# Performance work log

Measured on AMD Instinct MI355X. Metric: run time of the kernel, lower is better.

## Reference

```python
import math
import jax, jax.numpy as jnp
import numpy as np

EPS = 1e-6
MAX_SCALE_LOG = math.log(100.0)

def rms_norm(x, scale, eps=EPS):
    # x * scale / rms(x), reduction over last dim
    ms = jnp.mean(jnp.square(x), axis=-1, keepdims=True)
    return x * (scale * jax.lax.rsqrt(ms + eps))

def axial_rope_theta(pos, n_heads, d_head, dtype):
    # freqs: linspace in log-space from pi to 10*pi, reshaped to [n_heads, d_head//4]
    f = np.exp(np.linspace(math.log(math.pi), math.log(10.0 * math.pi),
                           n_heads * d_head // 4 + 1)[:-1])
    freqs = jnp.asarray(f.reshape(d_head // 4, n_heads).T, dtype)  # [h, e/4]
    theta_h = pos[:, :, None, 0:1] * freqs  # [n, l, h, e/4]
    theta_w = pos[:, :, None, 1:2] * freqs  # [n, l, h, e/4]
    theta = jnp.concatenate([theta_h, theta_w], axis=-1)  # [n, l, h, e/2]
    return theta.transpose(0, 2, 1, 3)  # [n, h, l, e/2]

def apply_rotary(x, theta):
    d = theta.shape[-1]
    x1, x2, x3 = x[..., :d], x[..., d:2 * d], x[..., 2 * d:]
    cos, sin = jnp.cos(theta), jnp.sin(theta)
    return jnp.concatenate([x1 * cos - x2 * sin, x2 * cos + x1 * sin, x3], axis=-1)

def setup_inputs() -> dict:
    key = jax.random.key(0)
    ks = jax.random.split(key, 8)
    n, l, d_model, d_head = 2, 2048, 1024, 64
    n_heads = d_model // d_head
    x = jax.random.normal(ks[0], (n, l, d_model), jnp.float32)
    pos = jax.random.uniform(ks[1], (n, l, 2), jnp.float32)
    cond = jax.random.normal(ks[2], (n, 1, d_model), jnp.float32)
    # params (torch uses zero-init for w_cond/w_out; small random for a non-degenerate baseline)
    w_cond = jax.random.normal(ks[3], (d_model, d_model), jnp.float32) * 0.02
    w_qkv = jax.random.normal(ks[4], (d_model, 3 * d_model), jnp.float32) * (d_model ** -0.5)
    qk_scale = jnp.full((n_heads,), math.log(10.0), jnp.float32)
    w_out = jax.random.normal(ks[5], (d_model, d_model), jnp.float32) * 0.02
    return {"x": x, "pos": pos, "cond": cond, "w_cond": w_cond,
            "w_qkv": w_qkv, "qk_scale": qk_scale, "w_out": w_out}

def reference(x, pos, cond, w_cond, w_qkv, qk_scale, w_out):
    n, l, d_model = x.shape
    h = qk_scale.shape[0]
    e = d_model // h
    # AdaRMSNorm: scale = linear(cond) + 1
    xn = rms_norm(x, cond @ w_cond + 1.0)
    # QKV projection
    q, k, v = jnp.split(xn @ w_qkv, 3, axis=-1)
    to_heads = lambda t: t.reshape(n, l, h, e).transpose(0, 2, 1, 3)  # [n,h,l,e]
    q, k, v = to_heads(q), to_heads(k), to_heads(v)
    # QKNorm: per-head learned scale, rms over head dim
    s = jnp.exp(0.5 * jnp.minimum(qk_scale, MAX_SCALE_LOG) - 0.25 * math.log(e))
    q = rms_norm(q, s[:, None, None])
    k = rms_norm(k, s[:, None, None])
    # Axial RoPE
    theta = axial_rope_theta(pos, h, e, x.dtype)
    q = apply_rotary(q, theta)
    k = apply_rotary(k, theta)
    # SDPA (no mask)
    attn = jax.nn.softmax(jnp.einsum('nhqe,nhke->nhqk', q, k) / math.sqrt(e), axis=-1)
    o = jnp.einsum('nhqk,nhke->nhqe', attn, v)
    o = o.transpose(0, 2, 1, 3).reshape(n, l, d_model)
    return o @ w_out
```

## Files before the change

kernel.cpp:

```cpp
#include <hip/hip_runtime.h>

typedef unsigned short u16;
typedef unsigned int u32;
typedef short s16x8 __attribute__((ext_vector_type(8)));
typedef short s16x4 __attribute__((ext_vector_type(4)));
typedef float f32x4 __attribute__((ext_vector_type(4)));
typedef u32 u32x2 __attribute__((ext_vector_type(2)));

#define AS1 __attribute__((address_space(1)))
#define AS3 __attribute__((address_space(3)))

__device__ __forceinline__ float bf2f(u16 u) {
    union { unsigned int i; float f; } x; x.i = ((unsigned int)u) << 16; return x.f;
}
__device__ __forceinline__ u16 f2bf(float f) {
    union { float f; unsigned int i; } x; x.f = f;
    unsigned int r = (x.i + 0x7FFFu + ((x.i >> 16) & 1u)) >> 16;
    return (u16)r;
}
__device__ __forceinline__ void storeOut(u16* p, float v) { *p = f2bf(v); }
__device__ __forceinline__ void storeOut(float* p, float v) { *p = v; }
__device__ __forceinline__ float loadIn(const void* p, size_t i, int isf32) {
    return isf32 ? ((const float*)p)[i] : bf2f(((const u16*)p)[i]);
}
__device__ __forceinline__ float fexp2(float x) {
#if __has_builtin(__builtin_amdgcn_exp2f)
    return __builtin_amdgcn_exp2f(x);
#else
    return exp2f(x);
#endif
}
__device__ __forceinline__ u32 pack_bf(float a, float b) {
    u32 ua = __float_as_uint(a) + 0x8000u;
    u32 ub = __float_as_uint(b) + 0x8000u;
    return __builtin_amdgcn_perm(ub, ua, 0x07060302u);
}

__global__ __launch_bounds__(256) void detect_dtype(const u16* __restrict__ x,
                                                    int* __restrict__ flag) {
    __shared__ int cnt[4];
    const int tid = threadIdx.x;
    int c = 0;
    #pragma unroll
    for (int i = 0; i < 4; ++i) {
        const u16 u = x[tid * 4 + i];
        const int e = (u >> 7) & 0xFF;
        c += (e >= 101 && e <= 135) ? 1 : 0;
    }
    #pragma unroll
    for (int m = 1; m < 64; m <<= 1) c += __shfl_xor(c, m, 64);
    if ((tid & 63) == 0) cnt[tid >> 6] = c;
    __syncthreads();
    if (tid == 0) {
        const int t = cnt[0] + cnt[1] + cnt[2] + cnt[3];
        *flag = (t < 800) ? 1 : 0;
    }
}

__global__ __launch_bounds__(256) void cond_gemv(const void* __restrict__ cond,
                                                 const void* __restrict__ w,
                                                 float* __restrict__ out,
                                                 const int* __restrict__ flag) {
    const int isf32 = *flag;
    const int d  = blockIdx.x * 256 + threadIdx.x;
    const int n  = blockIdx.y;
    const int k0 = blockIdx.z * 64;
    float acc = 0.f;
    #pragma unroll 8
    for (int k = 0; k < 64; ++k)
        acc += loadIn(cond, n * 1024 + k0 + k, isf32) *
               loadIn(w, (size_t)(k0 + k) * 1024 + d, isf32);
    atomicAdd(out + n * 1024 + d, acc);
}

__global__ __launch_bounds__(256) void rmsnorm_x(const void* __restrict__ x,
                                                 const float* __restrict__ scl,
                                                 u16* __restrict__ xn,
                                                 const int* __restrict__ flag) {
    const int isf32 = *flag;
    const int tok = blockIdx.x;
    const int n = tok >> 11;
    u16* orow = xn + (size_t)tok * 1024;
    const int base = threadIdx.x * 4;
    float f0, f1, f2, f3;
    if (isf32) {
        const float4 v = *(const float4*)((const float*)x + (size_t)tok * 1024 + base);
        f0 = v.x; f1 = v.y; f2 = v.z; f3 = v.w;
    } else {
        s16x4 uv = *(const s16x4*)((const u16*)x + (size_t)tok * 1024 + base);
        f0 = bf2f((u16)uv[0]); f1 = bf2f((u16)uv[1]); f2 = bf2f((u16)uv[2]); f3 = bf2f((u16)uv[3]);
    }
    float ss = f0 * f0 + f1 * f1 + f2 * f2 + f3 * f3;
    #pragma unroll
    for (int m = 1; m < 64; m <<= 1) ss += __shfl_xor(ss, m, 64);
    __shared__ float red[4];
    const int wave = threadIdx.x >> 6, lane = threadIdx.x & 63;
    if (lane == 0) red[wave] = ss;
    __syncthreads();
    float ms = (red[0] + red[1] + red[2] + red[3]) * (1.f / 1024.f);
    float rinv = rsqrtf(ms + 1e-6f);
    orow[base + 0] = f2bf(f0 * (scl[n * 1024 + base + 0] + 1.f) * rinv);
    orow[base + 1] = f2bf(f1 * (scl[n * 1024 + base + 1] + 1.f) * rinv);
    orow[base + 2] = f2bf(f2 * (scl[n * 1024 + base + 2] + 1.f) * rinv);
    orow[base + 3] = f2bf(f3 * (scl[n * 1024 + base + 3] + 1.f) * rinv);
}

__global__ __launch_bounds__(256) void transpose_bf(const void* __restrict__ src,
                                                    u16* __restrict__ dst, int R, int C,
                                                    const int* __restrict__ flag) {
    const int isf32 = *flag;
    __shared__ u16 t[32][33];
    const int c0 = blockIdx.x * 32, r0 = blockIdx.y * 32;
    const int tx = threadIdx.x & 31, ty = threadIdx.x >> 5;
    #pragma unroll
    for (int i = 0; i < 4; ++i)
        t[ty + i * 8][tx] = f2bf(loadIn(src, (size_t)(r0 + ty + i * 8) * C + c0 + tx, isf32));
    __syncthreads();
    #pragma unroll
    for (int i = 0; i < 4; ++i)
        dst[(size_t)(c0 + ty + i * 8) * R + r0 + tx] = t[tx][ty + i * 8];
}

template <typename OutT>
__global__ __launch_bounds__(256) void gemm_bt(const u16* __restrict__ A,
                                               const u16* __restrict__ BT,
                                               OutT* __restrict__ C, int Nn, int K) {
    __shared__ u16 As[128 * 32];
    __shared__ u16 Bs[128 * 32];
    const int tid = threadIdx.x;
    const int wave = tid >> 6, lane = tid & 63;
    const int l15 = lane & 15, quad = lane >> 4;
    const int bm0 = blockIdx.y * 128, bn0 = blockIdx.x * 128;
    const int wr = wave >> 1, wc = wave & 1;
    f32x4 acc[4][4] = {};
    const int srow = lane >> 2;
    const int g = (lane & 3) ^ (srow & 3);
    for (int bk = 0; bk < K; bk += 32) {
        __syncthreads();
        #pragma unroll
        for (int p = 0; p < 2; ++p) {
            const int rowl = p * 64 + wave * 16 + srow;
            __builtin_amdgcn_global_load_lds(
                (const AS1 void*)(A + (size_t)(bm0 + rowl) * K + bk + g * 8),
                (AS3 void*)(As + (p * 64 + wave * 16) * 32), 16, 0, 0);
            __builtin_amdgcn_global_load_lds(
                (const AS1 void*)(BT + (size_t)(bn0 + rowl) * K + bk + g * 8),
                (AS3 void*)(Bs + (p * 64 + wave * 16) * 32), 16, 0, 0);
        }
        __syncthreads();
        s16x8 af[4], bfr[4];
        #pragma unroll
        for (int mt = 0; mt < 4; ++mt) {
            const int r = wr * 64 + mt * 16 + l15;
            af[mt] = *(const s16x8*)(As + r * 32 + ((quad ^ (r & 3)) << 3));
        }
        #pragma unroll
        for (int nt = 0; nt < 4; ++nt) {
            const int r = wc * 64 + nt * 16 + l15;
            bfr[nt] = *(const s16x8*)(Bs + r * 32 + ((quad ^ (r & 3)) << 3));
        }
        #pragma unroll
        for (int mt = 0; mt < 4; ++mt)
            #pragma unroll
            for (int nt = 0; nt < 4; ++nt)
                acc[mt][nt] = __builtin_amdgcn_mfma_f32_16x16x32_bf16(af[mt], bfr[nt], acc[mt][nt], 0, 0, 0);
    }
    #pragma unroll
    for (int mt = 0; mt < 4; ++mt)
        #pragma unroll
        for (int nt = 0; nt < 4; ++nt)
            #pragma unroll
            for (int r = 0; r < 4; ++r) {
                const int row = bm0 + wr * 64 + mt * 16 + quad * 4 + r;
                const int col = bn0 + wc * 64 + nt * 16 + l15;
                storeOut(C + (size_t)row * Nn + col, acc[mt][nt][r]);
            }
}

template <typename OutT>
__global__ __launch_bounds__(256) void gemm_bt64(const u16* __restrict__ A,
                                                 const u16* __restrict__ BT,
                                                 OutT* __restrict__ C, int Nn, int K) {
    __shared__ u16 As[128 * 32];
    __shared__ u16 Bs[64 * 32];
    const int tid = threadIdx.x;
    const int wave = tid >> 6, lane = tid & 63;
    const int l15 = lane & 15, quad = lane >> 4;
    const int bm0 = blockIdx.y * 128, bn0 = blockIdx.x * 64;
    f32x4 acc[2][4] = {};
    const int srow = lane >> 2;
    const int g = (lane & 3) ^ (srow & 3);
    for (int bk = 0; bk < K; bk += 32) {
        __syncthreads();
        #pragma unroll
        for (int p = 0; p < 2; ++p) {
            const int rowl = p * 64 + wave * 16 + srow;
            __builtin_amdgcn_global_load_lds(
                (const AS1 void*)(A + (size_t)(bm0 + rowl) * K + bk + g * 8),
                (AS3 void*)(As + (p * 64 + wave * 16) * 32), 16, 0, 0);
        }
        {
            const int rowb = wave * 16 + srow;
            __builtin_amdgcn_global_load_lds(
                (const AS1 void*)(BT + (size_t)(bn0 + rowb) * K + bk + g * 8),
                (AS3 void*)(Bs + (wave * 16) * 32), 16, 0, 0);
        }
        __syncthreads();
        s16x8 af[2], bfr[4];
        #pragma unroll
        for (int mt = 0; mt < 2; ++mt) {
            const int r = wave * 32 + mt * 16 + l15;
            af[mt] = *(const s16x8*)(As + r * 32 + ((quad ^ (r & 3)) << 3));
        }
        #pragma unroll
        for (int nt = 0; nt < 4; ++nt) {
            const int r = nt * 16 + l15;
            bfr[nt] = *(const s16x8*)(Bs + r * 32 + ((quad ^ (r & 3)) << 3));
        }
        #pragma unroll
        for (int mt = 0; mt < 2; ++mt)
            #pragma unroll
            for (int nt = 0; nt < 4; ++nt)
                acc[mt][nt] = __builtin_amdgcn_mfma_f32_16x16x32_bf16(af[mt], bfr[nt], acc[mt][nt], 0, 0, 0);
    }
    #pragma unroll
    for (int mt = 0; mt < 2; ++mt)
        #pragma unroll
        for (int nt = 0; nt < 4; ++nt)
            #pragma unroll
            for (int r = 0; r < 4; ++r) {
                const int row = bm0 + wave * 32 + mt * 16 + quad * 4 + r;
                const int col = bn0 + nt * 16 + l15;
                storeOut(C + (size_t)row * Nn + col, acc[mt][nt][r]);
            }
}

__global__ __launch_bounds__(256) void qkv_head(const u16* __restrict__ qkv,
                                                const void* __restrict__ pos,
                                                const void* __restrict__ qk_scale,
                                                u16* __restrict__ q_ws,
                                                u16* __restrict__ k_ws,
                                                u16* __restrict__ vtg,
                                                const int* __restrict__ flag) {
    const int isf32 = *flag;
    const int nh = blockIdx.y;
    const int n = nh >> 4, h = nh & 15;
    const int l0 = blockIdx.x * 64;
    const int tid = threadIdx.x;
    const int wave = tid >> 6, lane = tid & 63;

    const float qs = loadIn(qk_scale, h, isf32);
    const float s = __expf(0.5f * fminf(qs, 4.605170186f) - 1.039720771f);
    const float qmul = s * s * 0.125f * 1.44269504089f;
    const int j = lane & 31;
    const float t = (float)((j & 15) * 16 + h);
    const float freq = 3.14159265358979f * __expf(t * (2.302585093f / 256.f));
    const int pj = j >> 4;

    #pragma unroll 2
    for (int it = 0; it < 16; ++it) {
        const int l = l0 + wave * 16 + it;
        const int tok = n * 2048 + l;
        const u16* row = qkv + (size_t)tok * 3072;
        float qv = bf2f(row[h * 64 + lane]);
        float kv = bf2f(row[1024 + h * 64 + lane]);
        float q2 = qv * qv, k2 = kv * kv;
        #pragma unroll
        for (int m = 1; m < 64; m <<= 1) { q2 += __shfl_xor(q2, m, 64); k2 += __shfl_xor(k2, m, 64); }
        float qn = qv * rsqrtf(q2 * (1.f / 64.f) + 1e-6f) * qmul;
        float kn = kv * rsqrtf(k2 * (1.f / 64.f) + 1e-6f);
        const float p = loadIn(pos, tok * 2 + pj, isf32);
        const float th = p * freq;
        const float c = __cosf(th), sn = __sinf(th);
        const float pq = __shfl_xor(qn, 32, 64);
        const float pk = __shfl_xor(kn, 32, 64);
        float qr, kr;
        if (lane < 32) { qr = qn * c - pq * sn; kr = kn * c - pk * sn; }
        else           { qr = qn * c + pq * sn; kr = kn * c + pk * sn; }
        const size_t oidx = ((size_t)nh * 2048 + l) * 64 + lane;
        q_ws[oidx] = f2bf(qr);
        k_ws[oidx] = f2bf(kr);
    }

    __shared__ u16 tbuf[64][65];
    const u16* vsrc = qkv + (size_t)(n * 2048 + l0) * 3072 + 2048 + h * 64;
    #pragma unroll
    for (int it = 0; it < 16; ++it) {
        const int idx = it * 256 + tid;
        const int r = idx >> 6, c = idx & 63;
        tbuf[r][c] = vsrc[(size_t)r * 3072 + c];
    }
    __syncthreads();
    u16* dst = vtg + (size_t)nh * 131072 + l0;
    #pragma unroll
    for (int it = 0; it < 16; ++it) {
        const int idx = it * 256 + tid;
        const int er = idx >> 6, lc = idx & 63;
        dst[(size_t)er * 2048 + lc] = tbuf[lc][er];
    }
}

__global__ __launch_bounds__(256, 3) void attn6(const u16* __restrict__ Q,
                                                const u16* __restrict__ K,
                                                const u16* __restrict__ Vtg,
                                                float* __restrict__ Opart,
                                                float* __restrict__ lpart) {
    __shared__ u16 Ks[2][64 * 64];
    __shared__ u16 Vt[2][64 * 64];
    __shared__ u16 Ps[4][32 * 72];
    const int nh = blockIdx.y;
    const int q0 = blockIdx.x * 128;
    const int ks = blockIdx.z;
    const int kb0 = ks * 1024;
    const int tid = threadIdx.x;
    const int wave = tid >> 6, lane = tid & 63;
    const int l15 = lane & 15, quad = lane >> 4;
    const size_t hb = (size_t)nh * 2048 * 64;
    const u16* Vbase = Vtg + (size_t)nh * 131072;
    const int dr0 = tid >> 3;
    const int dd  = tid & 7;

    s16x8 qf[2][2];
    #pragma unroll
    for (int qg = 0; qg < 2; ++qg)
        #pragma unroll
        for (int kc = 0; kc < 2; ++kc)
            qf[qg][kc] = *(const s16x8*)(Q + hb + (size_t)(q0 + wave * 32 + qg * 16 + l15) * 64 + kc * 32 + quad * 8);

    f32x4 Oacc[2][4] = {};
    float lacc[2] = {0.f, 0.f};
    u16* Pw = Ps[wave];

    #pragma unroll
    for (int it = 0; it < 2; ++it) {
        const int row = it * 32 + dr0;
        const int g = dd ^ (row & 7);
        __builtin_amdgcn_global_load_lds(
            (const AS1 void*)(K + hb + (size_t)(kb0 + row) * 64 + g * 8),
            (AS3 void*)(Ks[0] + (it * 256 + wave * 64) * 8), 16, 0, 0);
        __builtin_amdgcn_global_load_lds(
            (const AS1 void*)(Vbase + (size_t)row * 2048 + kb0 + g * 8),
            (AS3 void*)(Vt[0] + (it * 256 + wave * 64) * 8), 16, 0, 0);
    }
    __syncthreads();

    for (int i = 0; i < 16; ++i) {
        const int cur = i & 1;
        const int kb = kb0 + i * 64;
        if (i < 15) {
            const int nxt = cur ^ 1;
            const int kbn = kb + 64;
            #pragma unroll
            for (int it = 0; it < 2; ++it) {
                const int row = it * 32 + dr0;
                const int g = dd ^ (row & 7);
                __builtin_amdgcn_global_load_lds(
                    (const AS1 void*)(K + hb + (size_t)(kbn + row) * 64 + g * 8),
                    (AS3 void*)(Ks[nxt] + (it * 256 + wave * 64) * 8), 16, 0, 0);
                __builtin_amdgcn_global_load_lds(
                    (const AS1 void*)(Vbase + (size_t)row * 2048 + kbn + g * 8),
                    (AS3 void*)(Vt[nxt] + (it * 256 + wave * 64) * 8), 16, 0, 0);
            }
        }

        f32x4 S[2][4];
        #pragma unroll
        for (int qg = 0; qg < 2; ++qg)
            #pragma unroll
            for (int kt = 0; kt < 4; ++kt) {
                S[qg][kt][0] = -15.f; S[qg][kt][1] = -15.f;
                S[qg][kt][2] = -15.f; S[qg][kt][3] = -15.f;
            }
        #pragma unroll
        for (int kt = 0; kt < 4; ++kt) {
            const int r = kt * 16 + l15;
            #pragma unroll
            for (int kc = 0; kc < 2; ++kc) {
                const s16x8 kf = *(const s16x8*)(Ks[cur] + r * 64 + (((kc * 4 + quad) ^ (r & 7)) << 3));
                S[0][kt] = __builtin_amdgcn_mfma_f32_16x16x32_bf16(kf, qf[0][kc], S[0][kt], 0, 0, 0);
                S[1][kt] = __builtin_amdgcn_mfma_f32_16x16x32_bf16(kf, qf[1][kc], S[1][kt], 0, 0, 0);
            }
        }

        #pragma unroll
        for (int qg = 0; qg < 2; ++qg) {
            float rs = 0.f;
            #pragma unroll
            for (int kt = 0; kt < 4; ++kt) {
                const float e0 = fexp2(S[qg][kt][0]);
                const float e1 = fexp2(S[qg][kt][1]);
                const float e2 = fexp2(S[qg][kt][2]);
                const float e3 = fexp2(S[qg][kt][3]);
                rs += (e0 + e1) + (e2 + e3);
                u32x2 pk2;
                pk2[0] = pack_bf(e0, e1);
                pk2[1] = pack_bf(e2, e3);
                *(u32x2*)(Pw + (qg * 16 + l15) * 72 + kt * 16 + quad * 4) = pk2;
            }
            lacc[qg] += rs;
        }

        #pragma unroll
        for (int kc = 0; kc < 2; ++kc) {
            const s16x8 pf0 = *(const s16x8*)(Pw + l15 * 72 + kc * 32 + quad * 8);
            const s16x8 pf1 = *(const s16x8*)(Pw + (16 + l15) * 72 + kc * 32 + quad * 8);
            #pragma unroll
            for (int nto = 0; nto < 4; ++nto) {
                const int e = nto * 16 + l15;
                const s16x8 vf = *(const s16x8*)(Vt[cur] + e * 64 + (((kc * 4 + quad) ^ (e & 7)) << 3));
                Oacc[0][nto] = __builtin_amdgcn_mfma_f32_16x16x32_bf16(pf0, vf, Oacc[0][nto], 0, 0, 0);
                Oacc[1][nto] = __builtin_amdgcn_mfma_f32_16x16x32_bf16(pf1, vf, Oacc[1][nto], 0, 0, 0);
            }
        }

        if (i < 15) __syncthreads();
    }

    #pragma unroll
    for (int qg = 0; qg < 2; ++qg) {
        lacc[qg] += __shfl_xor(lacc[qg], 16, 64);
        lacc[qg] += __shfl_xor(lacc[qg], 32, 64);
    }

    const size_t pb = ((size_t)(ks * 32 + nh)) * 2048;
    if (quad == 0) {
        #pragma unroll
        for (int qg = 0; qg < 2; ++qg)
            lpart[pb + q0 + wave * 32 + qg * 16 + l15] = lacc[qg];
    }
    #pragma unroll
    for (int qg = 0; qg < 2; ++qg)
        #pragma unroll
        for (int r = 0; r < 4; ++r) {
            const int qrow = q0 + wave * 32 + qg * 16 + quad * 4 + r;
            float* orow = Opart + (pb + qrow) * 64;
            #pragma unroll
            for (int nto = 0; nto < 4; ++nto)
                orow[nto * 16 + l15] = Oacc[qg][nto][r];
        }
}

__global__ __launch_bounds__(256) void combine_o(const float* __restrict__ Opart,
                                                 const float* __restrict__ lpart,
                                                 u16* __restrict__ O) {
    constexpr size_t HS = (size_t)32 * 2048 * 64;
    constexpr size_t LS = (size_t)32 * 2048;
    const int tok = blockIdx.x;
    const int n = tok >> 11, l = tok & 2047;
    const int idx = threadIdx.x * 4;
    const int h = idx >> 6;
    const int nh = n * 16 + h;
    const size_t base = ((size_t)nh * 2048 + l) * 64 + (idx & 63);
    const float4 a = *(const float4*)(Opart + base);
    const float4 b = *(const float4*)(Opart + HS + base);
    const float inv = 1.f / (lpart[(size_t)nh * 2048 + l] + lpart[LS + (size_t)nh * 2048 + l]);
    u16* o = O + (size_t)tok * 1024 + idx;
    o[0] = f2bf((a.x + b.x) * inv);
    o[1] = f2bf((a.y + b.y) * inv);
    o[2] = f2bf((a.z + b.z) * inv);
    o[3] = f2bf((a.w + b.w) * inv);
}

extern "C" void kernel_launch(void* const* d_in, const int* in_sizes, int n_in,
                              void* d_out, int out_size, void* d_ws, size_t ws_size,
                              hipStream_t stream) {
    const void* x        = d_in[0];
    const void* pos      = d_in[1];
    const void* cond     = d_in[2];
    const void* w_cond   = d_in[3];
    const void* w_qkv    = d_in[4];
    const void* qk_scale = d_in[5];
    const void* w_out    = d_in[6];

    char* ws = (char*)d_ws;
    constexpr size_t MB = 1048576;
    constexpr size_t OFS_SCALE = 0;
    constexpr size_t OFS_FLAG  = 8192;
    constexpr size_t OFS_WOUTT = 16384;
    constexpr size_t OFS_Q     = OFS_WOUTT + 2 * MB;
    constexpr size_t OFS_K     = OFS_Q     + 8 * MB;
    constexpr size_t OFS_VT    = OFS_K     + 8 * MB;
    constexpr size_t OFS_O     = OFS_VT    + 8 * MB;
    constexpr size_t OFS_XN    = OFS_O     + 8 * MB;
    constexpr size_t OFS_WQKVT = OFS_XN    + 8 * MB;
    constexpr size_t OFS_QKV   = OFS_WQKVT + 6 * MB;
    constexpr size_t OFS_OPART = OFS_XN;
    constexpr size_t OFS_LPART = OFS_OPART + 32 * MB;

    float* scale = (float*)(ws + OFS_SCALE);
    int*   flag  = (int*)(ws + OFS_FLAG);
    u16* xn    = (u16*)(ws + OFS_XN);
    u16* wqkvT = (u16*)(ws + OFS_WQKVT);
    u16* woutT = (u16*)(ws + OFS_WOUTT);
    u16* qkv   = (u16*)(ws + OFS_QKV);
    u16* qws   = (u16*)(ws + OFS_Q);
    u16* kws   = (u16*)(ws + OFS_K);
    u16* vtg   = (u16*)(ws + OFS_VT);
    u16* ows   = (u16*)(ws + OFS_O);
    float* opart = (float*)(ws + OFS_OPART);
    float* lpart = (float*)(ws + OFS_LPART);

    detect_dtype<<<dim3(1), 256, 0, stream>>>((const u16*)x, flag);
    hipMemsetAsync(scale, 0, 2 * 1024 * sizeof(float), stream);
    cond_gemv<<<dim3(4, 2, 16), 256, 0, stream>>>(cond, w_cond, scale, flag);
    rmsnorm_x<<<dim3(4096), 256, 0, stream>>>(x, scale, xn, flag);
    transpose_bf<<<dim3(96, 32), 256, 0, stream>>>(w_qkv, wqkvT, 1024, 3072, flag);
    transpose_bf<<<dim3(32, 32), 256, 0, stream>>>(w_out, woutT, 1024, 1024, flag);
    gemm_bt<u16><<<dim3(24, 32), 256, 0, stream>>>(xn, wqkvT, qkv, 3072, 1024);
    qkv_head<<<dim3(32, 32), 256, 0, stream>>>(qkv, pos, qk_scale, qws, kws, vtg, flag);
    attn6<<<dim3(16, 32, 2), 256, 0, stream>>>(qws, kws, vtg, opart, lpart);
    combine_o<<<dim3(4096), 256, 0, stream>>>(opart, lpart, ows);
    gemm_bt64<float><<<dim3(16, 32), 256, 0, stream>>>(ows, woutT, (float*)d_out, 1024, 1024);
}
```

Measured before the change: 246.7 us.

## Double query rows per attention block and use 128-wide GEMM for output projection

The attention kernel now gives each wave 64 query rows instead of 32, so every K/V tile loaded into shared memory feeds twice as many MFMAs. The grid is halved and occupancy is lowered to 2 blocks per CU. The output projection drops the 128x64-tile GEMM in favour of the generic 128x128 gemm_bt kernel. The cost is more register pressure and fewer blocks: the attention launch goes to 512 blocks and the output GEMM to 256, which may underfill the GPU.

```diff
diff --git a/kernel.cpp b/kernel.cpp
--- a/kernel.cpp
+++ b/kernel.cpp
@@ -177,64 +177,6 @@
             }
 }
 
-template <typename OutT>
-__global__ __launch_bounds__(256) void gemm_bt64(const u16* __restrict__ A,
-                                                 const u16* __restrict__ BT,
-                                                 OutT* __restrict__ C, int Nn, int K) {
-    __shared__ u16 As[128 * 32];
-    __shared__ u16 Bs[64 * 32];
-    const int tid = threadIdx.x;
-    const int wave = tid >> 6, lane = tid & 63;
-    const int l15 = lane & 15, quad = lane >> 4;
-    const int bm0 = blockIdx.y * 128, bn0 = blockIdx.x * 64;
-    f32x4 acc[2][4] = {};
-    const int srow = lane >> 2;
-    const int g = (lane & 3) ^ (srow & 3);
-    for (int bk = 0; bk < K; bk += 32) {
-        __syncthreads();
-        #pragma unroll
-        for (int p = 0; p < 2; ++p) {
-            const int rowl = p * 64 + wave * 16 + srow;
-            __builtin_amdgcn_global_load_lds(
-                (const AS1 void*)(A + (size_t)(bm0 + rowl) * K + bk + g * 8),
-                (AS3 void*)(As + (p * 64 + wave * 16) * 32), 16, 0, 0);
-        }
-        {
-            const int rowb = wave * 16 + srow;
-            __builtin_amdgcn_global_load_lds(
-                (const AS1 void*)(BT + (size_t)(bn0 + rowb) * K + bk + g * 8),
-                (AS3 void*)(Bs + (wave * 16) * 32), 16, 0, 0);
-        }
-        __syncthreads();
-        s16x8 af[2], bfr[4];
-        #pragma unroll
-        for (int mt = 0; mt < 2; ++mt) {
-            const int r = wave * 32 + mt * 16 + l15;
-            af[mt] = *(const s16x8*)(As + r * 32 + ((quad ^ (r & 3)) << 3));
-        }
-        #pragma unroll
-        for (int nt = 0; nt < 4; ++nt) {
-            const int r = nt * 16 + l15;
-            bfr[nt] = *(const s16x8*)(Bs + r * 32 + ((quad ^ (r & 3)) << 3));
-        }
-        #pragma unroll
-        for (int mt = 0; mt < 2; ++mt)
-            #pragma unroll
-            for (int nt = 0; nt < 4; ++nt)
-                acc[mt][nt] = __builtin_amdgcn_mfma_f32_16x16x32_bf16(af[mt], bfr[nt], acc[mt][nt], 0, 0, 0);
-    }
-    #pragma unroll
-    for (int mt = 0; mt < 2; ++mt)
-        #pragma unroll
-        for (int nt = 0; nt < 4; ++nt)
-            #pragma unroll
-            for (int r = 0; r < 4; ++r) {
-                const int row = bm0 + wave * 32 + mt * 16 + quad * 4 + r;
-                const int col = bn0 + nt * 16 + l15;
-                storeOut(C + (size_t)row * Nn + col, acc[mt][nt][r]);
-            }
-}
-
 __global__ __launch_bounds__(256) void qkv_head(const u16* __restrict__ qkv,
                                                 const void* __restrict__ pos,
                                                 const void* __restrict__ qk_scale,
@@ -300,16 +242,16 @@
     }
 }
 
-__global__ __launch_bounds__(256, 3) void attn6(const u16* __restrict__ Q,
+__global__ __launch_bounds__(256, 2) void attn7(const u16* __restrict__ Q,
                                                 const u16* __restrict__ K,
                                                 const u16* __restrict__ Vtg,
                                                 float* __restrict__ Opart,
                                                 float* __restrict__ lpart) {
     __shared__ u16 Ks[2][64 * 64];
     __shared__ u16 Vt[2][64 * 64];
-    __shared__ u16 Ps[4][32 * 72];
+    __shared__ u16 Ps[4][64 * 72];
     const int nh = blockIdx.y;
-    const int q0 = blockIdx.x * 128;
+    const int q0 = blockIdx.x * 256;
     const int ks = blockIdx.z;
     const int kb0 = ks * 1024;
     const int tid = threadIdx.x;
@@ -320,15 +262,15 @@
     const int dr0 = tid >> 3;
     const int dd  = tid & 7;
 
-    s16x8 qf[2][2];
-    #pragma unroll
-    for (int qg = 0; qg < 2; ++qg)
+    s16x8 qf[4][2];
+    #pragma unroll
+    for (int qg = 0; qg < 4; ++qg)
         #pragma unroll
         for (int kc = 0; kc < 2; ++kc)
-            qf[qg][kc] = *(const s16x8*)(Q + hb + (size_t)(q0 + wave * 32 + qg * 16 + l15) * 64 + kc * 32 + quad * 8);
-
-    f32x4 Oacc[2][4] = {};
-    float lacc[2] = {0.f, 0.f};
+            qf[qg][kc] = *(const s16x8*)(Q + hb + (size_t)(q0 + wave * 64 + qg * 16 + l15) * 64 + kc * 32 + quad * 8);
+
+    f32x4 Oacc[4][4] = {};
+    float lacc[4] = {0.f, 0.f, 0.f, 0.f};
     u16* Pw = Ps[wave];
 
     #pragma unroll
@@ -363,9 +305,9 @@
             }
         }
 
-        f32x4 S[2][4];
-        #pragma unroll
-        for (int qg = 0; qg < 2; ++qg)
+        f32x4 S[4][4];
+        #pragma unroll
+        for (int qg = 0; qg < 4; ++qg)
             #pragma unroll
             for (int kt = 0; kt < 4; ++kt) {
                 S[qg][kt][0] = -15.f; S[qg][kt][1] = -15.f;
@@ -377,13 +319,14 @@
             #pragma unroll
             for (int kc = 0; kc < 2; ++kc) {
                 const s16x8 kf = *(const s16x8*)(Ks[cur] + r * 64 + (((kc * 4 + quad) ^ (r & 7)) << 3));
-                S[0][kt] = __builtin_amdgcn_mfma_f32_16x16x32_bf16(kf, qf[0][kc], S[0][kt], 0, 0, 0);
-                S[1][kt] = __builtin_amdgcn_mfma_f32_16x16x32_bf16(kf, qf[1][kc], S[1][kt], 0, 0, 0);
-            }
-        }
-
-        #pragma unroll
-        for (int qg = 0; qg < 2; ++qg) {
+                #pragma unroll
+                for (int qg = 0; qg < 4; ++qg)
+                    S[qg][kt] = __builtin_amdgcn_mfma_f32_16x16x32_bf16(kf, qf[qg][kc], S[qg][kt], 0, 0, 0);
+            }
+        }
+
+        #pragma unroll
+        for (int qg = 0; qg < 4; ++qg) {
             float rs = 0.f;
             #pragma unroll
             for (int kt = 0; kt < 4; ++kt) {
@@ -402,14 +345,17 @@
 
         #pragma unroll
         for (int kc = 0; kc < 2; ++kc) {
-            const s16x8 pf0 = *(const s16x8*)(Pw + l15 * 72 + kc * 32 + quad * 8);
-            const s16x8 pf1 = *(const s16x8*)(Pw + (16 + l15) * 72 + kc * 32 + quad * 8);
+            s16x8 pf[4];
+            #pragma unroll
+            for (int qg = 0; qg < 4; ++qg)
+                pf[qg] = *(const s16x8*)(Pw + (qg * 16 + l15) * 72 + kc * 32 + quad * 8);
             #pragma unroll
             for (int nto = 0; nto < 4; ++nto) {
                 const int e = nto * 16 + l15;
                 const s16x8 vf = *(const s16x8*)(Vt[cur] + e * 64 + (((kc * 4 + quad) ^ (e & 7)) << 3));
-                Oacc[0][nto] = __builtin_amdgcn_mfma_f32_16x16x32_bf16(pf0, vf, Oacc[0][nto], 0, 0, 0);
-                Oacc[1][nto] = __builtin_amdgcn_mfma_f32_16x16x32_bf16(pf1, vf, Oacc[1][nto], 0, 0, 0);
+                #pragma unroll
+                for (int qg = 0; qg < 4; ++qg)
+                    Oacc[qg][nto] = __builtin_amdgcn_mfma_f32_16x16x32_bf16(pf[qg], vf, Oacc[qg][nto], 0, 0, 0);
             }
         }
 
@@ -417,7 +363,7 @@
     }
 
     #pragma unroll
-    for (int qg = 0; qg < 2; ++qg) {
+    for (int qg = 0; qg < 4; ++qg) {
         lacc[qg] += __shfl_xor(lacc[qg], 16, 64);
         lacc[qg] += __shfl_xor(lacc[qg], 32, 64);
     }
@@ -425,14 +371,14 @@
     const size_t pb = ((size_t)(ks * 32 + nh)) * 2048;
     if (quad == 0) {
         #pragma unroll
-        for (int qg = 0; qg < 2; ++qg)
-            lpart[pb + q0 + wave * 32 + qg * 16 + l15] = lacc[qg];
-    }
-    #pragma unroll
-    for (int qg = 0; qg < 2; ++qg)
+        for (int qg = 0; qg < 4; ++qg)
+            lpart[pb + q0 + wave * 64 + qg * 16 + l15] = lacc[qg];
+    }
+    #pragma unroll
+    for (int qg = 0; qg < 4; ++qg)
         #pragma unroll
         for (int r = 0; r < 4; ++r) {
-            const int qrow = q0 + wave * 32 + qg * 16 + quad * 4 + r;
+            const int qrow = q0 + wave * 64 + qg * 16 + quad * 4 + r;
             float* orow = Opart + (pb + qrow) * 64;
             #pragma unroll
             for (int nto = 0; nto < 4; ++nto)
@@ -508,7 +454,7 @@
     transpose_bf<<<dim3(32, 32), 256, 0, stream>>>(w_out, woutT, 1024, 1024, flag);
     gemm_bt<u16><<<dim3(24, 32), 256, 0, stream>>>(xn, wqkvT, qkv, 3072, 1024);
     qkv_head<<<dim3(32, 32), 256, 0, stream>>>(qkv, pos, qk_scale, qws, kws, vtg, flag);
-    attn6<<<dim3(16, 32, 2), 256, 0, stream>>>(qws, kws, vtg, opart, lpart);
+    attn7<<<dim3(8, 32, 2), 256, 0, stream>>>(qws, kws, vtg, opart, lpart);
     combine_o<<<dim3(4096), 256, 0, stream>>>(opart, lpart, ows);
-    gemm_bt64<float><<<dim3(16, 32), 256, 0, stream>>>(ows, woutT, (float*)d_out, 1024, 1024);
-}
+    gemm_bt<float><<<dim3(8, 32), 256, 0, stream>>>(ows, woutT, (float*)d_out, 1024, 1024);
+}
```

New measurement: 248.2 us. About the same (+0.6%).
